# Optimization experiments

Measured on AMD Instinct MI355X. Metric: run time of the kernel, lower is better.

Reference implementation:

```python
import jax, jax.numpy as jnp
import numpy as np


def setup_inputs() -> dict:
    key = jax.random.key(0)
    ks = jax.random.split(key, 4)
    B, T, D, U = 32, 1024, 1024, 1024
    x = jax.random.normal(ks[0], (B, T, D), dtype=jnp.float32)
    W = jax.random.normal(ks[1], (D, 4 * U), dtype=jnp.float32) * (1.0 / np.sqrt(D))
    b = jnp.zeros((4 * U,), dtype=jnp.float32)
    Vr = jax.random.normal(ks[2], (U,), dtype=jnp.float32) * 0.1
    Vf = jax.random.normal(ks[3], (U,), dtype=jnp.float32) * 0.1
    h0 = jnp.zeros((B, U), dtype=jnp.float32)
    c0 = jnp.zeros((B, U), dtype=jnp.float32)
    return {"x": x, "h0": h0, "c0": c0, "W": W, "b": b, "Vr": Vr, "Vf": Vf}


def _sru(x, h0, c0, W, b, Vr, Vf):
    B, T, D = x.shape
    U = Vr.shape[0]
    # Batched matmul across all timesteps, then sequential elementwise scan.
    g = jnp.einsum('btd,dk->btk', x, W) + b            # [B, T, 4U]
    g = jnp.moveaxis(g, 1, 0)                          # [T, B, 4U]
    g1, g2, g3, g4 = jnp.split(g, 4, axis=-1)          # each [T, B, U]

    def step(c_, gs):
        a1, a2, a3, a4 = gs
        f = jax.nn.sigmoid(a1 + Vf * c_)
        c = f * c_ + (1.0 - f) * a2
        r = jax.nn.sigmoid(a3 + Vr * c_)
        h = r * c + (1.0 - r) * a4
        return c, h

    c_last, hs = jax.lax.scan(step, c0, (g1, g2, g3, g4))
    return jnp.moveaxis(hs, 0, 1)                      # [B, T, U]


def reference(x, h0, c0, W, b, Vr, Vf):
    return _sru(x, h0, c0, W, b, Vr, Vf)
```

## Files before the change

### kernel.cpp

```cpp
#include <hip/hip_runtime.h>
#include <cstdint>
#include <cstddef>

typedef short short8 __attribute__((ext_vector_type(8)));
typedef short s16x4 __attribute__((ext_vector_type(4)));
typedef float f32x4 __attribute__((ext_vector_type(4)));

typedef const __attribute__((address_space(1))) void* gas_ptr;
typedef __attribute__((address_space(3))) void* las_ptr;

__device__ __forceinline__ unsigned short f2bf(float f) {
    unsigned int u = __float_as_uint(f);
    u += 0x7fffu + ((u >> 16) & 1u);
    return (unsigned short)(u >> 16);
}
__device__ __forceinline__ float bf2f(unsigned short s) {
    return __uint_as_float(((unsigned int)s) << 16);
}
__device__ __forceinline__ float sigmoid_f(float z) {
    return __builtin_amdgcn_rcpf(1.0f + __expf(-z));
}
__device__ __forceinline__ void async_copy16(const void* gp, void* lp) {
    __builtin_amdgcn_global_load_lds((gas_ptr)gp, (las_ptr)lp, 16, 0, 0);
}

__global__ __launch_bounds__(256) void cvt_x_kernel(const float* __restrict__ in,
                                                    unsigned short* __restrict__ out) {
    size_t i = ((size_t)blockIdx.x * 256 + threadIdx.x) * 8;
    float4 v0 = *(const float4*)(in + i);
    float4 v1 = *(const float4*)(in + i + 4);
    short8 o;
    o[0]=(short)f2bf(v0.x); o[1]=(short)f2bf(v0.y); o[2]=(short)f2bf(v0.z); o[3]=(short)f2bf(v0.w);
    o[4]=(short)f2bf(v1.x); o[5]=(short)f2bf(v1.y); o[6]=(short)f2bf(v1.z); o[7]=(short)f2bf(v1.w);
    *(short8*)(out + i) = o;
}

__global__ __launch_bounds__(256) void cvt_w_kernel(const float* __restrict__ W,
                                                    unsigned short* __restrict__ Wt) {
    __shared__ unsigned short tile[64][65];
    int bk = blockIdx.x >> 6, bn = blockIdx.x & 63;
    int k0 = bk * 64, n0 = bn * 64;
    int t = threadIdx.x;
    int cr = t >> 6;
    int cc = t & 63;
#pragma unroll
    for (int i = 0; i < 16; ++i) {
        int row = i * 4 + cr;
        tile[row][cc] = f2bf(W[(size_t)(k0 + row) * 4096 + n0 + cc]);
    }
    __syncthreads();
#pragma unroll
    for (int i = 0; i < 16; ++i) {
        int nrow = i * 4 + cr;
        Wt[(size_t)(n0 + nrow) * 1024 + k0 + cc] = tile[cc][nrow];
    }
}

__global__ __launch_bounds__(256, 2) void gemm_kernel(const unsigned short* __restrict__ A,
                                                      const unsigned short* __restrict__ Bt,
                                                      const float* __restrict__ bias,
                                                      unsigned short* __restrict__ gT) {
    __shared__ __align__(16) unsigned short As[128 * 64];
    __shared__ __align__(16) unsigned short Bs[128 * 64];

    int bid = blockIdx.x;
    int band = bid >> 8;
    int r = bid & 255;
    int mt = band * 8 + (r >> 5);
    int nt = r & 31;
    int m0 = mt * 128, n0 = nt * 128;

    int tidx = threadIdx.x;
    int lane = tidx & 63, wv = tidx >> 6;
    int wm = wv >> 1, wn = wv & 1;
    int l15 = lane & 15, quad = lane >> 4;

    f32x4 acc[4][4] = {};

    for (int k0 = 0; k0 < 1024; k0 += 64) {
        __syncthreads();
#pragma unroll
        for (int i = 0; i < 4; ++i) {
            int ci = (wv * 4 + i) * 64 + lane;
            int row = ci >> 3, cc = ci & 7;
            int sc = (cc ^ (row & 7)) << 3;
            const unsigned short* ga = A + (size_t)(m0 + row) * 1024 + k0 + sc;
            async_copy16(ga, (char*)As + (wv * 4 + i) * 1024);
            const unsigned short* gb = Bt + (size_t)(n0 + row) * 1024 + k0 + sc;
            async_copy16(gb, (char*)Bs + (wv * 4 + i) * 1024);
        }
        __syncthreads();
#pragma unroll
        for (int kt = 0; kt < 2; ++kt) {
            short8 af[4], bf[4];
#pragma unroll
            for (int mt2 = 0; mt2 < 4; ++mt2) {
                int row = wm * 64 + mt2 * 16 + l15;
                int kc = kt * 4 + quad;
                af[mt2] = *(const short8*)((const char*)As + row * 128 + ((kc ^ (row & 7)) << 4));
            }
#pragma unroll
            for (int nt2 = 0; nt2 < 4; ++nt2) {
                int rown = wn * 64 + nt2 * 16 + l15;
                int kc = kt * 4 + quad;
                bf[nt2] = *(const short8*)((const char*)Bs + rown * 128 + ((kc ^ (rown & 7)) << 4));
            }
#pragma unroll
            for (int mt2 = 0; mt2 < 4; ++mt2)
#pragma unroll
                for (int nt2 = 0; nt2 < 4; ++nt2)
                    acc[mt2][nt2] = __builtin_amdgcn_mfma_f32_16x16x32_bf16(
                        af[mt2], bf[nt2], acc[mt2][nt2], 0, 0, 0);
        }
    }

#pragma unroll
    for (int mt2 = 0; mt2 < 4; ++mt2) {
        int mbase = m0 + wm * 64 + mt2 * 16 + quad * 4;
        int b_ = mbase >> 10, t_ = mbase & 1023;
#pragma unroll
        for (int nt2 = 0; nt2 < 4; ++nt2) {
            int n = n0 + wn * 64 + nt2 * 16 + l15;
            int gate = n >> 10, u = n & 1023;
            float bv = bias[n];
            s16x4 pk;
            pk[0] = (short)f2bf(acc[mt2][nt2][0] + bv);
            pk[1] = (short)f2bf(acc[mt2][nt2][1] + bv);
            pk[2] = (short)f2bf(acc[mt2][nt2][2] + bv);
            pk[3] = (short)f2bf(acc[mt2][nt2][3] + bv);
            *(s16x4*)(gT + (((size_t)(gate * 32 + b_) << 10) + (size_t)u) * 1024 + t_) = pk;
        }
    }
}

__global__ __launch_bounds__(64) void scan_kernel(const unsigned short* __restrict__ gT,
                                                  const float* __restrict__ c0,
                                                  const float* __restrict__ Vr,
                                                  const float* __restrict__ Vf,
                                                  float* __restrict__ h) {
    int tid = blockIdx.x * 64 + threadIdx.x;
    int b = tid >> 10, u = tid & 1023;
    const size_t GSTRIDE = (size_t)32 * 1024 * 1024;
    const unsigned short* p1 = gT + ((size_t)(b << 10) + u) * 1024;
    const unsigned short* p2 = p1 + GSTRIDE;
    const unsigned short* p3 = p2 + GSTRIDE;
    const unsigned short* p4 = p3 + GSTRIDE;
    float* hb = h + ((size_t)b << 20) + u;
    float c = c0[(b << 10) + u];
    float vf = Vf[u], vr = Vr[u];

    short8 r1[4], r2[4], r3[4], r4[4];
#pragma unroll
    for (int i = 0; i < 4; ++i) {
        r1[i] = *(const short8*)(p1 + i * 8);
        r2[i] = *(const short8*)(p2 + i * 8);
        r3[i] = *(const short8*)(p3 + i * 8);
        r4[i] = *(const short8*)(p4 + i * 8);
    }
    for (int tb = 0; tb < 1024; tb += 32) {
#pragma unroll
        for (int s = 0; s < 4; ++s) {
            short8 a1 = r1[s], a2 = r2[s], a3 = r3[s], a4 = r4[s];
            int tp = tb + 32 + s * 8;
            if (tp < 1024) {
                r1[s] = *(const short8*)(p1 + tp);
                r2[s] = *(const short8*)(p2 + tp);
                r3[s] = *(const short8*)(p3 + tp);
                r4[s] = *(const short8*)(p4 + tp);
            }
            int t0 = tb + s * 8;
#pragma unroll
            for (int i = 0; i < 8; ++i) {
                float x1 = bf2f((unsigned short)a1[i]);
                float x2 = bf2f((unsigned short)a2[i]);
                float x3 = bf2f((unsigned short)a3[i]);
                float x4 = bf2f((unsigned short)a4[i]);
                float f  = sigmoid_f(x1 + vf * c);
                float cn = fmaf(f, c - x2, x2);
                float rr = sigmoid_f(x3 + vr * c);
                float hv = fmaf(rr, cn - x4, x4);
                c = cn;
                hb[(size_t)(t0 + i) << 10] = hv;
            }
        }
    }
}

extern "C" void kernel_launch(void* const* d_in, const int* in_sizes, int n_in,
                              void* d_out, int out_size, void* d_ws, size_t ws_size,
                              hipStream_t stream) {
    const float* x  = (const float*)d_in[0];
    const float* c0 = (const float*)d_in[2];
    const float* W  = (const float*)d_in[3];
    const float* b  = (const float*)d_in[4];
    const float* Vr = (const float*)d_in[5];
    const float* Vf = (const float*)d_in[6];
    float* h = (float*)d_out;

    char* ws = (char*)d_ws;
    unsigned short* xb = (unsigned short*)ws;
    unsigned short* wt = (unsigned short*)(ws + (size_t)67108864);
    unsigned short* gT = (unsigned short*)(ws + (size_t)75497472);

    cvt_x_kernel<<<16384, 256, 0, stream>>>(x, xb);
    cvt_w_kernel<<<1024, 256, 0, stream>>>(W, wt);
    gemm_kernel<<<8192, 256, 0, stream>>>(xb, wt, b, gT);
    scan_kernel<<<512, 64, 0, stream>>>(gT, c0, Vr, Vf, h);
}
```

Baseline: 591.2 us.

## Tile gate buffer so scan wavefronts read coalesced 1KB chunks per timestep block

The GEMM epilogue now writes gates in a blocked layout [gate][b][u/64][t/8][u%64][t%8], so the 64 lanes of a scan wavefront read one contiguous 1KB block per 8 timesteps instead of 64 strided rows. The scan kernel's prefetch depth grows from 4 to 8 chunks, and h is written with nontemporal stores. This targets poor coalescing and latency in the memory-bound sequential scan. In exchange it uses more registers in the scan, and the GEMM epilogue stores become more scattered.

```diff
diff --git a/kernel.cpp b/kernel.cpp
--- a/kernel.cpp
+++ b/kernel.cpp
@@ -118,17 +118,21 @@
     for (int mt2 = 0; mt2 < 4; ++mt2) {
         int mbase = m0 + wm * 64 + mt2 * 16 + quad * 4;
         int b_ = mbase >> 10, t_ = mbase & 1023;
+        int tc = t_ >> 3, tt = t_ & 7;
 #pragma unroll
         for (int nt2 = 0; nt2 < 4; ++nt2) {
             int n = n0 + wn * 64 + nt2 * 16 + l15;
             int gate = n >> 10, u = n & 1023;
+            int ug = u >> 6, ul = u & 63;
             float bv = bias[n];
             s16x4 pk;
             pk[0] = (short)f2bf(acc[mt2][nt2][0] + bv);
             pk[1] = (short)f2bf(acc[mt2][nt2][1] + bv);
             pk[2] = (short)f2bf(acc[mt2][nt2][2] + bv);
             pk[3] = (short)f2bf(acc[mt2][nt2][3] + bv);
-            *(s16x4*)(gT + (((size_t)(gate * 32 + b_) << 10) + (size_t)u) * 1024 + t_) = pk;
+            size_t addr = ((((size_t)(gate * 32 + b_) * 16 + ug) * 128 + tc) * 512)
+                          + (size_t)(ul * 8 + tt);
+            *(s16x4*)(gT + addr) = pk;
         }
     }
 }
@@ -138,52 +142,60 @@
                                                   const float* __restrict__ Vr,
                                                   const float* __restrict__ Vf,
                                                   float* __restrict__ h) {
-    int tid = blockIdx.x * 64 + threadIdx.x;
+    int ul = threadIdx.x;
+    int tid = blockIdx.x * 64 + ul;
     int b = tid >> 10, u = tid & 1023;
-    const size_t GSTRIDE = (size_t)32 * 1024 * 1024;
-    const unsigned short* p1 = gT + ((size_t)(b << 10) + u) * 1024;
-    const unsigned short* p2 = p1 + GSTRIDE;
-    const unsigned short* p3 = p2 + GSTRIDE;
-    const unsigned short* p4 = p3 + GSTRIDE;
+    int ug = u >> 6;
+    const size_t PLANE = (size_t)33554432;
+    const unsigned short* p1 = gT + (((size_t)b * 16 + ug) * 128) * 512 + (size_t)(ul * 8);
+    const unsigned short* p2 = p1 + PLANE;
+    const unsigned short* p3 = p2 + PLANE;
+    const unsigned short* p4 = p3 + PLANE;
     float* hb = h + ((size_t)b << 20) + u;
     float c = c0[(b << 10) + u];
     float vf = Vf[u], vr = Vr[u];
 
-    short8 r1[4], r2[4], r3[4], r4[4];
-#pragma unroll
-    for (int i = 0; i < 4; ++i) {
-        r1[i] = *(const short8*)(p1 + i * 8);
-        r2[i] = *(const short8*)(p2 + i * 8);
-        r3[i] = *(const short8*)(p3 + i * 8);
-        r4[i] = *(const short8*)(p4 + i * 8);
-    }
-    for (int tb = 0; tb < 1024; tb += 32) {
-#pragma unroll
-        for (int s = 0; s < 4; ++s) {
-            short8 a1 = r1[s], a2 = r2[s], a3 = r3[s], a4 = r4[s];
-            int tp = tb + 32 + s * 8;
-            if (tp < 1024) {
-                r1[s] = *(const short8*)(p1 + tp);
-                r2[s] = *(const short8*)(p2 + tp);
-                r3[s] = *(const short8*)(p3 + tp);
-                r4[s] = *(const short8*)(p4 + tp);
-            }
-            int t0 = tb + s * 8;
-#pragma unroll
-            for (int i = 0; i < 8; ++i) {
-                float x1 = bf2f((unsigned short)a1[i]);
-                float x2 = bf2f((unsigned short)a2[i]);
-                float x3 = bf2f((unsigned short)a3[i]);
-                float x4 = bf2f((unsigned short)a4[i]);
-                float f  = sigmoid_f(x1 + vf * c);
-                float cn = fmaf(f, c - x2, x2);
-                float rr = sigmoid_f(x3 + vr * c);
-                float hv = fmaf(rr, cn - x4, x4);
-                c = cn;
-                hb[(size_t)(t0 + i) << 10] = hv;
-            }
-        }
-    }
+    short8 r1[8], r2[8], r3[8], r4[8];
+#pragma unroll
+    for (int j = 0; j < 8; ++j) {
+        r1[j] = *(const short8*)(p1 + (size_t)j * 512);
+        r2[j] = *(const short8*)(p2 + (size_t)j * 512);
+        r3[j] = *(const short8*)(p3 + (size_t)j * 512);
+        r4[j] = *(const short8*)(p4 + (size_t)j * 512);
+    }
+
+#define SRU_CHUNK(TC, PREFETCH)                                                \
+    {                                                                          \
+        int s_ = (TC) & 7;                                                     \
+        short8 a1 = r1[s_], a2 = r2[s_], a3 = r3[s_], a4 = r4[s_];             \
+        if (PREFETCH) {                                                        \
+            size_t off_ = (size_t)((TC) + 8) * 512;                            \
+            r1[s_] = *(const short8*)(p1 + off_);                              \
+            r2[s_] = *(const short8*)(p2 + off_);                              \
+            r3[s_] = *(const short8*)(p3 + off_);                              \
+            r4[s_] = *(const short8*)(p4 + off_);                              \
+        }                                                                      \
+        int t0_ = (TC) * 8;                                                    \
+        _Pragma("unroll")                                                      \
+        for (int i = 0; i < 8; ++i) {                                          \
+            float x1 = bf2f((unsigned short)a1[i]);                            \
+            float x2 = bf2f((unsigned short)a2[i]);                            \
+            float x3 = bf2f((unsigned short)a3[i]);                            \
+            float x4 = bf2f((unsigned short)a4[i]);                            \
+            float f  = sigmoid_f(x1 + vf * c);                                 \
+            float cn = fmaf(f, c - x2, x2);                                    \
+            float rr = sigmoid_f(x3 + vr * c);                                 \
+            float hv = fmaf(rr, cn - x4, x4);                                  \
+            c = cn;                                                            \
+            __builtin_nontemporal_store(hv, &hb[(size_t)(t0_ + i) << 10]);     \
+        }                                                                      \
+    }
+
+#pragma unroll 8
+    for (int tc = 0; tc < 120; ++tc) SRU_CHUNK(tc, 1)
+#pragma unroll
+    for (int tc = 120; tc < 128; ++tc) SRU_CHUNK(tc, 0)
+#undef SRU_CHUNK
 }
 
 extern "C" void kernel_launch(void* const* d_in, const int* in_sizes, int n_in,
```

Result: no change. 598.7 us (+1.3%).
